# Kernel optimization log

Hardware: AMD Instinct MI355X
Metric: run time of the kernel (lower is better)

The kernel has to match this reference:

```python
import jax, jax.numpy as jnp
import numpy as np


def _params_to_tokens(params):
    # (batch, 2k) -> (batch, k, 2) : chunk into freqs/amps then stack
    freqs, amps = jnp.split(params, 2, axis=-1)
    return jnp.stack((freqs, amps), axis=-1)


def setup_inputs() -> dict:
    key = jax.random.key(0)
    k1, k2 = jax.random.split(key)
    predicted = jax.random.normal(k1, (64, 4096), dtype=jnp.float32)
    target = jax.random.normal(k2, (64, 4096), dtype=jnp.float32)
    return {"predicted": predicted, "target": target}


def reference(predicted, target):
    p = _params_to_tokens(predicted)   # (b, k, 2)
    t = _params_to_tokens(target)      # (b, k, 2)
    # Euclidean cdist via gram-matrix identity (avoids (b,k,k,2) broadcast temp)
    p2 = jnp.sum(p * p, axis=-1)       # (b, k)
    t2 = jnp.sum(t * t, axis=-1)       # (b, k)
    gram = jnp.einsum('bid,bjd->bij', p, t)  # (b, k, k)
    sq = p2[:, :, None] + t2[:, None, :] - 2.0 * gram
    costs = jnp.sqrt(jnp.maximum(sq, 0.0))   # (b, k, k)
    min1 = jnp.mean(jnp.min(costs, axis=1), axis=-1)  # min over predicted dim
    min2 = jnp.mean(jnp.min(costs, axis=2), axis=-1)  # min over target dim
    return jnp.mean(min1 + min2)
```

## Files before the change

kernel.cpp:

```cpp
#include <hip/hip_runtime.h>


typedef _Float16 f16;
typedef _Float16 f16x8 __attribute__((ext_vector_type(8)));
typedef float f32x16 __attribute__((ext_vector_type(16)));

constexpr int K = 2048;
constexpr int BLOCK = 512;
constexpr int NBAND = 8;
constexpr int BAND = 256;
constexpr int NJT = K / 32;
constexpr unsigned INF_U = 0x7F800000u;

#define MFMA16 __builtin_amdgcn_mfma_f32_32x32x16_f16

__device__ __forceinline__ unsigned pk(f16 lo, f16 hi) {
  unsigned a = (unsigned)__builtin_bit_cast(unsigned short, lo);
  unsigned b = (unsigned)__builtin_bit_cast(unsigned short, hi);
  return a | (b << 16);
}
__device__ __forceinline__ unsigned split2(float v) {
  const f16 h = (f16)v;
  const f16 l = (f16)(v - (float)h);
  return pk(h, l);
}
__device__ __forceinline__ float min3p(float a, float b, float c) {
  return fminf(fminf(a, b), c);
}

__device__ __forceinline__ void colfold(const f32x16& d, unsigned* addr) {
  const float t0 = min3p(d[0], d[1], d[2]);
  const float t1 = min3p(d[3], d[4], d[5]);
  const float t2 = min3p(d[6], d[7], d[8]);
  const float t3 = min3p(d[9], d[10], d[11]);
  const float t4 = min3p(d[12], d[13], d[14]);
  float cm = fminf(min3p(t0, t1, t2), min3p(t3, t4, d[15]));
  cm = fmaxf(cm, 0.0f);
  atomicMin(addr, __float_as_uint(cm));
}

__global__ __launch_bounds__(BLOCK, 6) void chamfer_mfma(
    const float* __restrict__ pred, const float* __restrict__ targ,
    float* __restrict__ out, float* __restrict__ ws) {
  const int iband = blockIdx.x;
  const int b = blockIdx.y;
  const int tid = threadIdx.x;
  const int lane = tid & 63;
  const int w = tid >> 6;
  const int r = lane & 31;
  const bool lo_half = (lane < 32);

  __shared__ uint4 BrecP[K + 1];
  __shared__ uint4 ArecP[2 * BAND];
  __shared__ unsigned colmin_u[K];
  __shared__ float wsum[8];

  const float* tb = targ + (size_t)b * (2 * K);
  const float* pb = pred + (size_t)b * (2 * K);

  #pragma unroll
  for (int k = 0; k < K / BLOCK; ++k) {
    const int j = tid + k * BLOCK;
    const float x = tb[j], y = tb[K + j];
    const unsigned wx = split2(x);
    const unsigned wy = split2(y);
    const unsigned wt = split2(fmaf(x, x, y * y));
    BrecP[j] = make_uint4(wx,
                          (wx & 0xffffu) | (wy << 16),
                          (wy >> 16) | (wy << 16),
                          wt);
    colmin_u[j] = INF_U;
  }
  if (tid == 0) BrecP[K] = make_uint4(0x3C003C00u, 0u, 0u, 0u);
  if (tid < BAND) {
    const int i = iband * BAND + tid;
    const float x = pb[i], y = pb[K + i];
    const unsigned wu = split2(-2.0f * x);
    const unsigned ww = split2(-2.0f * y);
    const unsigned wp = split2(fmaf(x, x, y * y));
    ArecP[tid] = make_uint4((wu & 0xffffu) | (wu << 16),
                            (wu >> 16) | (ww << 16),
                            ww,
                            0x3C003C00u);
    ArecP[BAND + tid] = make_uint4(wp, 0u, 0u, 0u);
  }
  __syncthreads();

  const f32x16 zero = {};

  const f16x8 af = __builtin_bit_cast(
      f16x8, ArecP[(lo_half ? 0 : BAND) + w * 32 + r]);

  f32x16 rowacc;
  #pragma unroll
  for (int q = 0; q < 16; ++q) rowacc[q] = 3.4e38f;

  int bidx = lo_half ? r : (int)K;
  const int bstep = lo_half ? 32 : 0;

  uint4 c0 = BrecP[bidx];
  uint4 c1 = BrecP[bidx + bstep];
  bidx += 2 * bstep;

  #pragma unroll 1
  for (int jt = 0; jt < NJT - 2; jt += 2) {
    const uint4 n0 = BrecP[bidx];
    const uint4 n1 = BrecP[bidx + bstep];
    bidx += 2 * bstep;

    const f32x16 d0 = MFMA16(af, __builtin_bit_cast(f16x8, c0), zero, 0, 0, 0);
    const f32x16 d1 = MFMA16(af, __builtin_bit_cast(f16x8, c1), zero, 0, 0, 0);

    #pragma unroll
    for (int q = 0; q < 16; ++q)
      rowacc[q] = min3p(rowacc[q], d0[q], d1[q]);

    colfold(d0, &colmin_u[jt * 32 + r]);
    colfold(d1, &colmin_u[jt * 32 + 32 + r]);

    c0 = n0;
    c1 = n1;
  }
  {
    const int jt = NJT - 2;
    const f32x16 d0 = MFMA16(af, __builtin_bit_cast(f16x8, c0), zero, 0, 0, 0);
    const f32x16 d1 = MFMA16(af, __builtin_bit_cast(f16x8, c1), zero, 0, 0, 0);
    #pragma unroll
    for (int q = 0; q < 16; ++q)
      rowacc[q] = min3p(rowacc[q], d0[q], d1[q]);
    colfold(d0, &colmin_u[jt * 32 + r]);
    colfold(d1, &colmin_u[jt * 32 + 32 + r]);
  }

  #pragma unroll
  for (int m = 1; m <= 16; m <<= 1) {
    #pragma unroll
    for (int q = 0; q < 16; ++q)
      rowacc[q] = fminf(rowacc[q], __shfl_xor(rowacc[q], m, 64));
  }
  float s = 0.0f;
  #pragma unroll
  for (int q = 0; q < 16; ++q) s += sqrtf(fmaxf(rowacc[q], 0.0f));
  s += __shfl_xor(s, 32, 64);
  if (lane == 0) wsum[w] = s;
  __syncthreads();
  if (tid == 0) {
    float t = 0.0f;
    #pragma unroll
    for (int i = 0; i < 8; ++i) t += wsum[i];
    atomicAdd(out, t * (1.0f / 131072.0f));
  }
  float* wrow = ws + (size_t)(b * NBAND + iband) * K;
  #pragma unroll
  for (int k = 0; k < K / BLOCK; ++k) {
    const int j = tid + k * BLOCK;
    wrow[j] = __uint_as_float(colmin_u[j]);
  }
}

__global__ __launch_bounds__(256, 4) void chamfer_pass2(
    const float* __restrict__ ws, float* __restrict__ out) {
  const int b = blockIdx.x;
  const int tid = threadIdx.x;
  __shared__ float wsum[4];
  const float* wrow = ws + (size_t)b * NBAND * K;
  float s = 0.0f;
  #pragma unroll
  for (int k = 0; k < K / 256; ++k) {
    const int j = tid + k * 256;
    float m = wrow[j];
    #pragma unroll
    for (int band = 1; band < NBAND; ++band) m = fminf(m, wrow[band * K + j]);
    s += sqrtf(m);
  }
  #pragma unroll
  for (int off = 32; off; off >>= 1) s += __shfl_down(s, off, 64);
  const int lane = tid & 63, w = tid >> 6;
  if (lane == 0) wsum[w] = s;
  __syncthreads();
  if (tid == 0)
    atomicAdd(out, (wsum[0] + wsum[1] + wsum[2] + wsum[3]) * (1.0f / 131072.0f));
}

extern "C" void kernel_launch(void* const* d_in, const int* in_sizes, int n_in,
                              void* d_out, int out_size, void* d_ws, size_t ws_size,
                              hipStream_t stream) {
  const float* pred = (const float*)d_in[0];
  const float* targ = (const float*)d_in[1];
  float* out = (float*)d_out;
  float* ws = (float*)d_ws;

  dim3 g1(NBAND, 64);
  chamfer_mfma<<<g1, dim3(BLOCK), 0, stream>>>(pred, targ, out, ws);
  chamfer_pass2<<<dim3(64), dim3(256), 0, stream>>>(ws, out);
}
```

Baseline: 80.16 us.

## Give each wave two A tiles over half the columns to halve column atomics

Each wave now holds two 32-row A fragments and sweeps half of the target columns, where before it held one fragment and swept all of them. This reuses each loaded B fragment across two MFMAs and merges the two results before one atomicMin per column tile, halving the LDS atomic traffic. Row minima from the two column halves are combined through LDS scratch and reduced with DPP instead of shuffles. While those waves reduce, the other half of the block writes the column minima out with vector stores, and pass2 is split across four times as many blocks. Holding two accumulators raises register pressure, so the launch bound drops to 4 waves per SIMD.

```diff
diff --git a/kernel.cpp b/kernel.cpp
--- a/kernel.cpp
+++ b/kernel.cpp
@@ -9,10 +9,17 @@
 constexpr int BLOCK = 512;
 constexpr int NBAND = 8;
 constexpr int BAND = 256;
-constexpr int NJT = K / 32;
+constexpr int JW = 32;
 constexpr unsigned INF_U = 0x7F800000u;
 
 #define MFMA16 __builtin_amdgcn_mfma_f32_32x32x16_f16
+
+#define DPP_MIN(m, ctrl)                                                   \
+  {                                                                        \
+    int _i = __builtin_bit_cast(int, m);                                   \
+    int _r = __builtin_amdgcn_update_dpp(_i, _i, (ctrl), 0xF, 0xF, false); \
+    m = fminf(m, __builtin_bit_cast(float, _r));                           \
+  }
 
 __device__ __forceinline__ unsigned pk(f16 lo, f16 hi) {
   unsigned a = (unsigned)__builtin_bit_cast(unsigned short, lo);
@@ -28,18 +35,7 @@
   return fminf(fminf(a, b), c);
 }
 
-__device__ __forceinline__ void colfold(const f32x16& d, unsigned* addr) {
-  const float t0 = min3p(d[0], d[1], d[2]);
-  const float t1 = min3p(d[3], d[4], d[5]);
-  const float t2 = min3p(d[6], d[7], d[8]);
-  const float t3 = min3p(d[9], d[10], d[11]);
-  const float t4 = min3p(d[12], d[13], d[14]);
-  float cm = fminf(min3p(t0, t1, t2), min3p(t3, t4, d[15]));
-  cm = fmaxf(cm, 0.0f);
-  atomicMin(addr, __float_as_uint(cm));
-}
-
-__global__ __launch_bounds__(BLOCK, 6) void chamfer_mfma(
+__global__ __launch_bounds__(BLOCK, 4) void chamfer_mfma(
     const float* __restrict__ pred, const float* __restrict__ targ,
     float* __restrict__ out, float* __restrict__ ws) {
   const int iband = blockIdx.x;
@@ -47,13 +43,15 @@
   const int tid = threadIdx.x;
   const int lane = tid & 63;
   const int w = tid >> 6;
+  const int ip = w & 3;
+  const int jh = w >> 2;
   const int r = lane & 31;
   const bool lo_half = (lane < 32);
 
   __shared__ uint4 BrecP[K + 1];
   __shared__ uint4 ArecP[2 * BAND];
   __shared__ unsigned colmin_u[K];
-  __shared__ float wsum[8];
+  __shared__ float wtot;
 
   const float* tb = targ + (size_t)b * (2 * K);
   const float* pb = pred + (size_t)b * (2 * K);
@@ -88,86 +86,121 @@
 
   const f32x16 zero = {};
 
-  const f16x8 af = __builtin_bit_cast(
-      f16x8, ArecP[(lo_half ? 0 : BAND) + w * 32 + r]);
-
-  f32x16 rowacc;
-  #pragma unroll
-  for (int q = 0; q < 16; ++q) rowacc[q] = 3.4e38f;
-
-  int bidx = lo_half ? r : (int)K;
+  const int abase = lo_half ? 0 : BAND;
+  const f16x8 af0 = __builtin_bit_cast(f16x8, ArecP[abase + (2 * ip) * 32 + r]);
+  const f16x8 af1 = __builtin_bit_cast(f16x8, ArecP[abase + (2 * ip + 1) * 32 + r]);
+
+  f32x16 rowacc0, rowacc1;
+  #pragma unroll
+  for (int q = 0; q < 16; ++q) { rowacc0[q] = 3.4e38f; rowacc1[q] = 3.4e38f; }
+
+  int bidx = lo_half ? (jh * JW * 32 + r) : (int)K;
   const int bstep = lo_half ? 32 : 0;
-
-  uint4 c0 = BrecP[bidx];
-  uint4 c1 = BrecP[bidx + bstep];
-  bidx += 2 * bstep;
-
+  const int cbase = jh * JW * 32 + r;
+
+  auto compute = [&](const uint4& q4, int it) {
+    const f32x16 d0 = MFMA16(af0, __builtin_bit_cast(f16x8, q4), zero, 0, 0, 0);
+    const f32x16 d1 = MFMA16(af1, __builtin_bit_cast(f16x8, q4), zero, 0, 0, 0);
+    #pragma unroll
+    for (int q = 0; q < 16; ++q) rowacc0[q] = fminf(rowacc0[q], d0[q]);
+    #pragma unroll
+    for (int q = 0; q < 16; ++q) rowacc1[q] = fminf(rowacc1[q], d1[q]);
+    float mm[16];
+    #pragma unroll
+    for (int q = 0; q < 16; ++q) mm[q] = fminf(d0[q], d1[q]);
+    const float a0 = min3p(mm[0], mm[1], mm[2]);
+    const float a1 = min3p(mm[3], mm[4], mm[5]);
+    const float a2 = min3p(mm[6], mm[7], mm[8]);
+    const float a3 = min3p(mm[9], mm[10], mm[11]);
+    const float a4 = min3p(mm[12], mm[13], mm[14]);
+    float cm = fminf(min3p(a0, a1, a2), min3p(a3, a4, mm[15]));
+    cm = fmaxf(cm, 0.0f);
+    atomicMin(&colmin_u[cbase + it * 32], __float_as_uint(cm));
+  };
+
+  uint4 cq = BrecP[bidx];
+  bidx += bstep;
   #pragma unroll 1
-  for (int jt = 0; jt < NJT - 2; jt += 2) {
-    const uint4 n0 = BrecP[bidx];
-    const uint4 n1 = BrecP[bidx + bstep];
-    bidx += 2 * bstep;
-
-    const f32x16 d0 = MFMA16(af, __builtin_bit_cast(f16x8, c0), zero, 0, 0, 0);
-    const f32x16 d1 = MFMA16(af, __builtin_bit_cast(f16x8, c1), zero, 0, 0, 0);
-
-    #pragma unroll
-    for (int q = 0; q < 16; ++q)
-      rowacc[q] = min3p(rowacc[q], d0[q], d1[q]);
-
-    colfold(d0, &colmin_u[jt * 32 + r]);
-    colfold(d1, &colmin_u[jt * 32 + 32 + r]);
-
-    c0 = n0;
-    c1 = n1;
-  }
-  {
-    const int jt = NJT - 2;
-    const f32x16 d0 = MFMA16(af, __builtin_bit_cast(f16x8, c0), zero, 0, 0, 0);
-    const f32x16 d1 = MFMA16(af, __builtin_bit_cast(f16x8, c1), zero, 0, 0, 0);
-    #pragma unroll
-    for (int q = 0; q < 16; ++q)
-      rowacc[q] = min3p(rowacc[q], d0[q], d1[q]);
-    colfold(d0, &colmin_u[jt * 32 + r]);
-    colfold(d1, &colmin_u[jt * 32 + 32 + r]);
-  }
-
-  #pragma unroll
-  for (int m = 1; m <= 16; m <<= 1) {
-    #pragma unroll
-    for (int q = 0; q < 16; ++q)
-      rowacc[q] = fminf(rowacc[q], __shfl_xor(rowacc[q], m, 64));
-  }
-  float s = 0.0f;
-  #pragma unroll
-  for (int q = 0; q < 16; ++q) s += sqrtf(fmaxf(rowacc[q], 0.0f));
-  s += __shfl_xor(s, 32, 64);
-  if (lane == 0) wsum[w] = s;
-  __syncthreads();
-  if (tid == 0) {
-    float t = 0.0f;
-    #pragma unroll
-    for (int i = 0; i < 8; ++i) t += wsum[i];
-    atomicAdd(out, t * (1.0f / 131072.0f));
-  }
-  float* wrow = ws + (size_t)(b * NBAND + iband) * K;
-  #pragma unroll
-  for (int k = 0; k < K / BLOCK; ++k) {
-    const int j = tid + k * BLOCK;
-    wrow[j] = __uint_as_float(colmin_u[j]);
-  }
+  for (int it = 0; it < JW - 1; ++it) {
+    const uint4 nq = BrecP[bidx];
+    bidx += bstep;
+    compute(cq, it);
+    cq = nq;
+  }
+  compute(cq, JW - 1);
+
+  __syncthreads();
+
+  float* scratch = (float*)BrecP;
+  if (w >= 4) {
+    #pragma unroll
+    for (int t = 0; t < 2; ++t) {
+      float* dst = scratch + (((w - 4) * 2 + t) * 64 + lane) * 16;
+      const f32x16& ra = t ? rowacc1 : rowacc0;
+      #pragma unroll
+      for (int k = 0; k < 4; ++k) {
+        *(float4*)(dst + 4 * k) =
+            make_float4(ra[4 * k], ra[4 * k + 1], ra[4 * k + 2], ra[4 * k + 3]);
+      }
+    }
+  }
+  if (tid == 0) wtot = 0.0f;
+  __syncthreads();
+
+  if (w < 4) {
+    #pragma unroll
+    for (int t = 0; t < 2; ++t) {
+      f32x16& ra = t ? rowacc1 : rowacc0;
+      const float* src = scratch + ((w * 2 + t) * 64 + lane) * 16;
+      #pragma unroll
+      for (int k = 0; k < 4; ++k) {
+        const float4 v = *(const float4*)(src + 4 * k);
+        ra[4 * k]     = fminf(ra[4 * k], v.x);
+        ra[4 * k + 1] = fminf(ra[4 * k + 1], v.y);
+        ra[4 * k + 2] = fminf(ra[4 * k + 2], v.z);
+        ra[4 * k + 3] = fminf(ra[4 * k + 3], v.w);
+      }
+    }
+    #pragma unroll
+    for (int q = 0; q < 16; ++q) {
+      float m0 = rowacc0[q], m1 = rowacc1[q];
+      DPP_MIN(m0, 0x111); DPP_MIN(m0, 0x112); DPP_MIN(m0, 0x114);
+      DPP_MIN(m0, 0x118); DPP_MIN(m0, 0x142);
+      DPP_MIN(m1, 0x111); DPP_MIN(m1, 0x112); DPP_MIN(m1, 0x114);
+      DPP_MIN(m1, 0x118); DPP_MIN(m1, 0x142);
+      rowacc0[q] = m0; rowacc1[q] = m1;
+    }
+    if (lane == 31 || lane == 63) {
+      float s = 0.0f;
+      #pragma unroll
+      for (int q = 0; q < 16; ++q) {
+        s += sqrtf(fmaxf(rowacc0[q], 0.0f)) + sqrtf(fmaxf(rowacc1[q], 0.0f));
+      }
+      atomicAdd(&wtot, s);
+    }
+  } else {
+    float* wrow = ws + (size_t)(b * NBAND + iband) * K;
+    const int t2 = tid & 255;
+    const uint4 c0 = *(const uint4*)&colmin_u[t2 * 8];
+    const uint4 c1 = *(const uint4*)&colmin_u[t2 * 8 + 4];
+    *(uint4*)&wrow[t2 * 8] = c0;
+    *(uint4*)&wrow[t2 * 8 + 4] = c1;
+  }
+  __syncthreads();
+  if (tid == 0) atomicAdd(out, wtot * (1.0f / 131072.0f));
 }
 
 __global__ __launch_bounds__(256, 4) void chamfer_pass2(
     const float* __restrict__ ws, float* __restrict__ out) {
-  const int b = blockIdx.x;
+  const int b = blockIdx.x >> 2;
+  const int qt = blockIdx.x & 3;
   const int tid = threadIdx.x;
   __shared__ float wsum[4];
   const float* wrow = ws + (size_t)b * NBAND * K;
   float s = 0.0f;
   #pragma unroll
-  for (int k = 0; k < K / 256; ++k) {
-    const int j = tid + k * 256;
+  for (int k = 0; k < 2; ++k) {
+    const int j = qt * 512 + k * 256 + tid;
     float m = wrow[j];
     #pragma unroll
     for (int band = 1; band < NBAND; ++band) m = fminf(m, wrow[band * K + j]);
@@ -192,5 +225,5 @@
 
   dim3 g1(NBAND, 64);
   chamfer_mfma<<<g1, dim3(BLOCK), 0, stream>>>(pred, targ, out, ws);
-  chamfer_pass2<<<dim3(64), dim3(256), 0, stream>>>(ws, out);
-}
+  chamfer_pass2<<<dim3(256), dim3(256), 0, stream>>>(ws, out);
+}
```

New measurement: 102.5 us. 1.28x slower.
